# Performance work log

Measured on AMD Instinct MI355X. Metric: run time of the kernel, lower is better.

## Reference

```python
import jax, jax.numpy as jnp
import numpy as np

B, N, NFEAT = 32, 512, 256
NHID, NHEADS, NOUT = 64, 8, 128
ALPHA = 0.2    # GraphAttn LeakyReLU slope
ACVT_SLOPE = 0.01  # default nn.LeakyReLU slope in GAT.acvt
EPS = 1e-12


def _leaky(x, slope):
    return jnp.where(x >= 0, x, slope * x)


def setup_inputs() -> dict:
    key = jax.random.key(0)
    ks = jax.random.split(key, 10)
    s = lambda fan_in: 1.0 / np.sqrt(fan_in)
    return {
        "batch_descs": jax.random.normal(ks[0], (B, N, NFEAT), dtype=jnp.float32),
        # per-head GraphAttn params (nn.Linear weights, no bias)
        "W_tran": jax.random.uniform(ks[1], (NHEADS, NHID, NFEAT), jnp.float32, -s(NFEAT), s(NFEAT)),
        "a1": jax.random.uniform(ks[2], (NHEADS, NHID), jnp.float32, -s(NHID), s(NHID)),
        "a2": jax.random.uniform(ks[3], (NHEADS, NHID), jnp.float32, -s(NHID), s(NHID)),
        # output GraphAttn: in = NHID*NHEADS, out = NOUT
        "W_out": jax.random.uniform(ks[4], (NOUT, NHID * NHEADS), jnp.float32, -s(NHID * NHEADS), s(NHID * NHEADS)),
        "a1_out": jax.random.uniform(ks[5], (NOUT,), jnp.float32, -s(NOUT), s(NOUT)),
        "a2_out": jax.random.uniform(ks[6], (NOUT,), jnp.float32, -s(NOUT), s(NOUT)),
        # final nn.Linear(nout, nout) with bias
        "W_lin": jax.random.uniform(ks[7], (NOUT, NOUT), jnp.float32, -s(NOUT), s(NOUT)),
        "b_lin": jax.random.uniform(ks[8], (NOUT,), jnp.float32, -s(NOUT), s(NOUT)),
    }


def reference(batch_descs, W_tran, a1, a2, W_out, a1_out, a2_out, W_lin, b_lin):
    def gat_one_object(x):  # x: [N, NFEAT]; dense all-ones adj (ignored by GraphAttn)
        # ---- multi-head GraphAttn ----
        h = jnp.einsum('nf,hdf->hnd', x, W_tran)          # [H, N, NHID]
        e1 = jnp.einsum('hnd,hd->hn', h, a1)              # [H, N]
        e2 = jnp.einsum('hnd,hd->hn', h, a2)              # [H, N]
        # e[h, j, k] = a1(h_k) + a2(h_j); softmax over k (torch dim=1 on [N,N])
        e = _leaky(e1[:, None, :] + e2[:, :, None], ALPHA)  # [H, N, N]
        att = jax.nn.softmax(e, axis=-1)
        o = jnp.einsum('hjk,hkd->hjd', att, h)            # [H, N, NHID]
        o = jnp.transpose(o, (1, 0, 2)).reshape(N, NHEADS * NHID)  # concat heads
        # ---- acvt (dropout2 is identity in eval) ----
        x2 = _leaky(o, ACVT_SLOPE)
        # ---- output GraphAttn ----
        h2 = x2 @ W_out.T                                 # [N, NOUT]
        f1 = h2 @ a1_out                                  # [N]
        f2 = h2 @ a2_out                                  # [N]
        e_o = _leaky(f1[None, :] + f2[:, None], ALPHA)    # [N, N]
        att_o = jax.nn.softmax(e_o, axis=-1)
        out = att_o @ h2                                  # [N, NOUT]
        out = jnp.mean(out, axis=0)                       # [NOUT]
        return out @ W_lin.T + b_lin

    feats = jax.vmap(gat_one_object)(batch_descs)         # [B, NOUT]
    # F.normalize(p=2, dim=-1) with eps clamp
    norm = jnp.maximum(jnp.linalg.norm(feats, axis=-1, keepdims=True), EPS)
    return feats / norm
```

## Files before the change

### kernel.cpp

```cpp
#include <hip/hip_runtime.h>
#include <hip/hip_bf16.h>
#include <math.h>

#define BB 32
#define NN 512
#define NF 256
#define NHID 64
#define NHEADS_ 8
#define NO 128
#define ALPHA 0.2f
#define ACVT 0.01f

typedef __attribute__((ext_vector_type(8))) __bf16 bf16x8;
typedef __attribute__((ext_vector_type(4))) __bf16 bf16x4;
typedef __attribute__((ext_vector_type(4))) float f32x4;

__global__ __launch_bounds__(256) void cvt_k(const float* __restrict__ X,
                                             const float* __restrict__ Wt,
                                             const float* __restrict__ Wo,
                                             __bf16* __restrict__ Xb,
                                             __bf16* __restrict__ Wtb,
                                             __bf16* __restrict__ Wob) {
    int u = blockIdx.x * 256 + threadIdx.x;
    const float* src;
    __bf16* dst;
    int idx;
    if (u < 524288) { src = X; dst = Xb; idx = u; }
    else if (u < 540672) { src = Wt; dst = Wtb; idx = u - 524288; }
    else { src = Wo; dst = Wob; idx = u - 540672; }
    float4 v0 = *(const float4*)(src + (size_t)idx * 8);
    float4 v1 = *(const float4*)(src + (size_t)idx * 8 + 4);
    bf16x8 o;
    o[0] = (__bf16)v0.x; o[1] = (__bf16)v0.y; o[2] = (__bf16)v0.z; o[3] = (__bf16)v0.w;
    o[4] = (__bf16)v1.x; o[5] = (__bf16)v1.y; o[6] = (__bf16)v1.z; o[7] = (__bf16)v1.w;
    *(bf16x8*)(dst + (size_t)idx * 8) = o;
}

__global__ __launch_bounds__(256) void gemm1_bf16(
    const __bf16* __restrict__ Xb, const __bf16* __restrict__ Wtb,
    __bf16* __restrict__ HT,
    const float* __restrict__ a1, const float* __restrict__ a2,
    float* __restrict__ E1, float* __restrict__ E2) {
    __shared__ char As[128 * 128];
    __shared__ char Bs[128 * 128];
    const int tid = threadIdx.x;
    const int w = tid >> 6, lane = tid & 63;
    const int wm = w >> 1, wn = w & 1;
    const int r = lane & 15, g = lane >> 4;
    const int m0 = blockIdx.x * 128;
    const int n0 = blockIdx.y * 128;

    f32x4 acc[4][4];
#pragma unroll
    for (int mt = 0; mt < 4; ++mt)
#pragma unroll
        for (int nt = 0; nt < 4; ++nt) {
            acc[mt][nt][0] = 0.f; acc[mt][nt][1] = 0.f;
            acc[mt][nt][2] = 0.f; acc[mt][nt][3] = 0.f;
        }

    const int sr = tid >> 3;
    const int sc = (tid & 7) * 16;

    for (int k0 = 0; k0 < 256; k0 += 64) {
        __syncthreads();
#pragma unroll
        for (int i = 0; i < 4; ++i) {
            int row = sr + i * 32;
            bf16x8 va = *(const bf16x8*)((const char*)Xb +
                                         ((size_t)(m0 + row) * 256 + k0) * 2 + sc);
            *(bf16x8*)(As + row * 128 + (sc ^ ((row & 7) << 4))) = va;
            bf16x8 vb = *(const bf16x8*)((const char*)Wtb +
                                         ((size_t)(n0 + row) * 256 + k0) * 2 + sc);
            *(bf16x8*)(Bs + row * 128 + (sc ^ ((row & 7) << 4))) = vb;
        }
        __syncthreads();
#pragma unroll
        for (int kk = 0; kk < 64; kk += 32) {
            bf16x8 af[4], bfv[4];
#pragma unroll
            for (int mt = 0; mt < 4; ++mt) {
                int row = wm * 64 + mt * 16 + r;
                af[mt] = *(const bf16x8*)(As + row * 128 +
                                          (((kk + g * 8) * 2) ^ ((row & 7) << 4)));
            }
#pragma unroll
            for (int nt = 0; nt < 4; ++nt) {
                int row = wn * 64 + nt * 16 + r;
                bfv[nt] = *(const bf16x8*)(Bs + row * 128 +
                                           (((kk + g * 8) * 2) ^ ((row & 7) << 4)));
            }
#pragma unroll
            for (int mt = 0; mt < 4; ++mt)
#pragma unroll
                for (int nt = 0; nt < 4; ++nt)
                    acc[mt][nt] = __builtin_amdgcn_mfma_f32_16x16x32_bf16(
                        af[mt], bfv[nt], acc[mt][nt], 0, 0, 0);
        }
    }

    const int h = blockIdx.y * 2 + wn;
#pragma unroll
    for (int mt = 0; mt < 4; ++mt) {
        int mfirst = m0 + wm * 64 + mt * 16 + g * 4;
        int b = mfirst >> 9, nn = mfirst & 511;
#pragma unroll
        for (int nt = 0; nt < 4; ++nt) {
            int d = wn * 64 + nt * 16 + r - wn * 64;
            bf16x4 pv;
#pragma unroll
            for (int reg = 0; reg < 4; ++reg) pv[reg] = (__bf16)acc[mt][nt][reg];
            *(bf16x4*)(HT + ((size_t)(b * 8 + h) * 64 + d) * 512 + nn) = pv;
        }
    }
    float w1[4], w2[4];
#pragma unroll
    for (int nt = 0; nt < 4; ++nt) {
        w1[nt] = a1[h * 64 + nt * 16 + r];
        w2[nt] = a2[h * 64 + nt * 16 + r];
    }
#pragma unroll
    for (int mt = 0; mt < 4; ++mt)
#pragma unroll
        for (int reg = 0; reg < 4; ++reg) {
            float s1 = 0.f, s2 = 0.f;
#pragma unroll
            for (int nt = 0; nt < 4; ++nt) {
                s1 += acc[mt][nt][reg] * w1[nt];
                s2 += acc[mt][nt][reg] * w2[nt];
            }
#pragma unroll
            for (int off = 1; off <= 8; off <<= 1) {
                s1 += __shfl_xor(s1, off, 64);
                s2 += __shfl_xor(s2, off, 64);
            }
            if (r == 0) {
                int m = m0 + wm * 64 + mt * 16 + g * 4 + reg;
                int b = m >> 9, n = m & 511;
                E1[(size_t)(b * 8 + h) * 512 + n] = s1;
                E2[(size_t)(b * 8 + h) * 512 + n] = s2;
            }
        }
}

__global__ __launch_bounds__(256) void attn_mfma(const __bf16* __restrict__ HT,
                                                 const float* __restrict__ E1,
                                                 const float* __restrict__ E2,
                                                 __bf16* __restrict__ OL) {
    __shared__ char Ht[64 * 1024];
    __shared__ float e1s[512];
    __shared__ float red[4][64];
    __shared__ float e1maxS;

    const int bid = blockIdx.x;
    const int bh = bid >> 1, half = bid & 1;
    const int b = bh >> 3, h = bh & 7;
    const int tid = threadIdx.x;
    const int w = tid >> 6, lane = tid & 63;
    const int r = lane & 15, g = lane >> 4;

    {
        const char* src = (const char*)(HT + (size_t)bh * 32768);
#pragma unroll
        for (int i = 0; i < 16; ++i) {
            int off = i * 4096 + tid * 16;
            int d = off >> 10;
            bf16x8 v = *(const bf16x8*)(src + off);
            *(bf16x8*)(Ht + (off ^ ((d & 7) << 4))) = v;
        }
    }
    for (int i = tid; i < 512; i += 256) e1s[i] = E1[(size_t)bh * 512 + i];
    __syncthreads();

    ((float*)red)[tid] = fmaxf(e1s[tid], e1s[tid + 256]);
    __syncthreads();
    if (tid < 64) {
        const float* rp = (const float*)red;
        float m = fmaxf(fmaxf(rp[tid], rp[tid + 64]), fmaxf(rp[tid + 128], rp[tid + 192]));
#pragma unroll
        for (int off = 32; off >= 1; off >>= 1) m = fmaxf(m, __shfl_xor(m, off, 64));
        if (tid == 0) e1maxS = m;
    }
    __syncthreads();
    const float e1max = e1maxS;

    float ee2[4], mm[4];
    const float* e2g = E2 + (size_t)bh * 512 + half * 256 + w * 64;
#pragma unroll
    for (int mt = 0; mt < 4; ++mt) {
        float v = e2g[mt * 16 + r];
        ee2[mt] = v;
        float s = e1max + v;
        mm[mt] = fmaxf(s, ALPHA * s);
    }

    f32x4 acc[4][4];
#pragma unroll
    for (int mt = 0; mt < 4; ++mt)
#pragma unroll
        for (int nt = 0; nt < 4; ++nt) {
            acc[mt][nt][0] = 0.f; acc[mt][nt][1] = 0.f;
            acc[mt][nt][2] = 0.f; acc[mt][nt][3] = 0.f;
        }
    float zac[4] = {0.f, 0.f, 0.f, 0.f};

    for (int c = 0; c < 16; ++c) {
        const float* ep = e1s + c * 32 + g * 8;
        float4 ea = *(const float4*)(ep);
        float4 eb = *(const float4*)(ep + 4);
        float e1c[8] = {ea.x, ea.y, ea.z, ea.w, eb.x, eb.y, eb.z, eb.w};

        bf16x8 bfr[4];
#pragma unroll
        for (int nt = 0; nt < 4; ++nt) {
            int n = nt * 16 + r;
            int off = (n << 10) + ((c * 32 + g * 8) << 1);
            off ^= (n & 7) << 4;
            bfr[nt] = *(const bf16x8*)(Ht + off);
        }
#pragma unroll
        for (int mt = 0; mt < 4; ++mt) {
            bf16x8 af;
            float zp = 0.f;
#pragma unroll
            for (int q = 0; q < 8; ++q) {
                float s = e1c[q] + ee2[mt];
                s = fmaxf(s, ALPHA * s);
                float p = __expf(s - mm[mt]);
                zp += p;
                af[q] = (__bf16)p;
            }
            zac[mt] += zp;
#pragma unroll
            for (int nt = 0; nt < 4; ++nt)
                acc[mt][nt] =
                    __builtin_amdgcn_mfma_f32_16x16x32_bf16(af, bfr[nt], acc[mt][nt], 0, 0, 0);
        }
    }

#pragma unroll
    for (int mt = 0; mt < 4; ++mt) {
        float z = zac[mt];
        z += __shfl_xor(z, 16, 64);
        z += __shfl_xor(z, 32, 64);
        if (g == 0) red[w][mt * 16 + r] = 1.f / z;
    }

    __bf16* ob = OL + ((size_t)b * 512 + half * 256 + w * 64) * 512 + h * 64;
#pragma unroll
    for (int mt = 0; mt < 4; ++mt) {
#pragma unroll
        for (int reg = 0; reg < 4; ++reg) {
            int row = mt * 16 + g * 4 + reg;
            float zi = red[w][row];
#pragma unroll
            for (int nt = 0; nt < 4; ++nt) {
                float v = acc[mt][nt][reg] * zi;
                v = fmaxf(v, ACVT * v);
                ob[(size_t)row * 512 + nt * 16 + r] = (__bf16)v;
            }
        }
    }
}

__global__ __launch_bounds__(256) void gemm2_bf16(
    const __bf16* __restrict__ OL, const __bf16* __restrict__ Wob,
    float* __restrict__ H2,
    const float* __restrict__ a1o, const float* __restrict__ a2o,
    float* __restrict__ F1, float* __restrict__ F2) {
    __shared__ char As[32 * 128];
    __shared__ char Bs[128 * 128];
    __shared__ float fred[2][32][2];
    const int tid = threadIdx.x;
    const int w = tid >> 6, lane = tid & 63;
    const int wm = w >> 1, wn = w & 1;
    const int r = lane & 15, g = lane >> 4;
    const int m0 = blockIdx.x * 32;

    f32x4 acc[4];
#pragma unroll
    for (int nt = 0; nt < 4; ++nt) {
        acc[nt][0] = 0.f; acc[nt][1] = 0.f; acc[nt][2] = 0.f; acc[nt][3] = 0.f;
    }

    const int sra = tid >> 3;
    const int sc = (tid & 7) * 16;

    for (int k0 = 0; k0 < 512; k0 += 64) {
        __syncthreads();
        {
            bf16x8 va = *(const bf16x8*)((const char*)OL +
                                         ((size_t)(m0 + sra) * 512 + k0) * 2 + sc);
            *(bf16x8*)(As + sra * 128 + (sc ^ ((sra & 7) << 4))) = va;
        }
#pragma unroll
        for (int i = 0; i < 4; ++i) {
            int row = sra + i * 32;
            bf16x8 vb = *(const bf16x8*)((const char*)Wob +
                                         ((size_t)row * 512 + k0) * 2 + sc);
            *(bf16x8*)(Bs + row * 128 + (sc ^ ((row & 7) << 4))) = vb;
        }
        __syncthreads();
#pragma unroll
        for (int kk = 0; kk < 64; kk += 32) {
            int arow = wm * 16 + r;
            bf16x8 af = *(const bf16x8*)(As + arow * 128 +
                                         (((kk + g * 8) * 2) ^ ((arow & 7) << 4)));
            bf16x8 bfv[4];
#pragma unroll
            for (int nt = 0; nt < 4; ++nt) {
                int row = wn * 64 + nt * 16 + r;
                bfv[nt] = *(const bf16x8*)(Bs + row * 128 +
                                           (((kk + g * 8) * 2) ^ ((row & 7) << 4)));
            }
#pragma unroll
            for (int nt = 0; nt < 4; ++nt)
                acc[nt] = __builtin_amdgcn_mfma_f32_16x16x32_bf16(af, bfv[nt], acc[nt], 0, 0, 0);
        }
    }

#pragma unroll
    for (int reg = 0; reg < 4; ++reg) {
        int row = m0 + wm * 16 + g * 4 + reg;
#pragma unroll
        for (int nt = 0; nt < 4; ++nt)
            H2[(size_t)row * 128 + wn * 64 + nt * 16 + r] = acc[nt][reg];
    }
    float w1[4], w2[4];
#pragma unroll
    for (int nt = 0; nt < 4; ++nt) {
        w1[nt] = a1o[wn * 64 + nt * 16 + r];
        w2[nt] = a2o[wn * 64 + nt * 16 + r];
    }
#pragma unroll
    for (int reg = 0; reg < 4; ++reg) {
        float s1 = 0.f, s2 = 0.f;
#pragma unroll
        for (int nt = 0; nt < 4; ++nt) {
            s1 += acc[nt][reg] * w1[nt];
            s2 += acc[nt][reg] * w2[nt];
        }
#pragma unroll
        for (int off = 1; off <= 8; off <<= 1) {
            s1 += __shfl_xor(s1, off, 64);
            s2 += __shfl_xor(s2, off, 64);
        }
        if (r == 0) {
            int lr = wm * 16 + g * 4 + reg;
            fred[wn][lr][0] = s1;
            fred[wn][lr][1] = s2;
        }
    }
    __syncthreads();
    if (tid < 32) {
        int m = m0 + tid;
        int b = m >> 9, n = m & 511;
        F1[(size_t)b * 512 + n] = fred[0][tid][0] + fred[1][tid][0];
        F2[(size_t)b * 512 + n] = fred[0][tid][1] + fred[1][tid][1];
    }
}

__global__ __launch_bounds__(256) void zw_k(const float* __restrict__ F1,
                                            const float* __restrict__ F2,
                                            float* __restrict__ WP) {
    __shared__ float f1s[512];
    __shared__ float wpart[4][512];
    __shared__ float redm[256];
    const int b = blockIdx.x >> 4, jc = blockIdx.x & 15;
    const int tid = threadIdx.x;
    const int w = tid >> 6, lane = tid & 63;

    f1s[tid] = F1[(size_t)b * 512 + tid];
    f1s[tid + 256] = F1[(size_t)b * 512 + tid + 256];
#pragma unroll
    for (int i = 0; i < 8; ++i) wpart[w][lane + 64 * i] = 0.f;
    __syncthreads();
    redm[tid] = fmaxf(f1s[tid], f1s[tid + 256]);
    __syncthreads();
    if (tid < 64) {
        float m = fmaxf(fmaxf(redm[tid], redm[tid + 64]), fmaxf(redm[tid + 128], redm[tid + 192]));
#pragma unroll
        for (int off = 32; off >= 1; off >>= 1) m = fmaxf(m, __shfl_xor(m, off, 64));
        if (tid == 0) redm[0] = m;
    }
    __syncthreads();
    const float f1m = redm[0];

    for (int jj = 0; jj < 8; ++jj) {
        int j = jc * 32 + w * 8 + jj;
        float f2j = F2[(size_t)b * 512 + j];
        float sj = f1m + f2j;
        float mj = fmaxf(sj, ALPHA * sj);
        float pv[8];
        float z = 0.f;
#pragma unroll
        for (int i = 0; i < 8; ++i) {
            float s = f1s[lane + 64 * i] + f2j;
            s = fmaxf(s, ALPHA * s);
            float p = __expf(s - mj);
            pv[i] = p;
            z += p;
        }
#pragma unroll
        for (int off = 32; off >= 1; off >>= 1) z += __shfl_xor(z, off, 64);
        float inv = 1.f / z;
#pragma unroll
        for (int i = 0; i < 8; ++i) wpart[w][lane + 64 * i] += pv[i] * inv;
    }
    __syncthreads();
    for (int i = tid; i < 512; i += 256)
        WP[(size_t)(b * 16 + jc) * 512 + i] =
            wpart[0][i] + wpart[1][i] + wpart[2][i] + wpart[3][i];
}

__global__ __launch_bounds__(256) void vpart_k(const float* __restrict__ WP,
                                               const float* __restrict__ H2,
                                               float* __restrict__ VP) {
    __shared__ float wsL[128];
    const int b = blockIdx.x, kq = blockIdx.y;
    const int tid = threadIdx.x;
    if (tid < 128) {
        float s = 0.f;
#pragma unroll
        for (int jc = 0; jc < 16; ++jc) s += WP[(size_t)(b * 16 + jc) * 512 + kq * 128 + tid];
        wsL[tid] = s;
    }
    __syncthreads();
    const int d = tid & 127, half = tid >> 7;
    const float* h2p = H2 + ((size_t)b * 512 + kq * 128 + half * 64) * 128 + d;
    float acc = 0.f;
#pragma unroll 8
    for (int i = 0; i < 64; ++i) acc += wsL[half * 64 + i] * h2p[(size_t)i * 128];
    VP[(size_t)(b * 8 + kq * 2 + half) * 128 + d] = acc;
}

__global__ __launch_bounds__(256) void final3_k(const float* __restrict__ VP,
                                                const float* __restrict__ Wl,
                                                const float* __restrict__ bl,
                                                float* __restrict__ out) {
    __shared__ float vs[128];
    __shared__ float fo_s[128];
    __shared__ float r0;
    const int b = blockIdx.x, tid = threadIdx.x;
    if (tid < 128) {
        float v = 0.f;
#pragma unroll
        for (int q = 0; q < 8; ++q) v += VP[(size_t)(b * 8 + q) * 128 + tid];
        vs[tid] = v * (1.f / 512.f);
    }
    __syncthreads();
    if (tid < 128) {
        float fo = bl[tid];
        const float* wl = Wl + (size_t)tid * 128;
#pragma unroll 4
        for (int d = 0; d < 128; d += 4)
            fo += vs[d] * wl[d] + vs[d + 1] * wl[d + 1] + vs[d + 2] * wl[d + 2] +
                  vs[d + 3] * wl[d + 3];
        fo_s[tid] = fo;
    }
    __syncthreads();
    if (tid < 64) {
        float s = fo_s[tid] * fo_s[tid] + fo_s[tid + 64] * fo_s[tid + 64];
#pragma unroll
        for (int off = 32; off >= 1; off >>= 1) s += __shfl_xor(s, off, 64);
        if (tid == 0) r0 = s;
    }
    __syncthreads();
    float inv = 1.f / fmaxf(sqrtf(r0), 1e-12f);
    if (tid < 128) out[(size_t)b * 128 + tid] = fo_s[tid] * inv;
}

extern "C" void kernel_launch(void* const* d_in, const int* in_sizes, int n_in,
                              void* d_out, int out_size, void* d_ws, size_t ws_size,
                              hipStream_t stream) {
    const float* X = (const float*)d_in[0];
    const float* Wt = (const float*)d_in[1];
    const float* a1 = (const float*)d_in[2];
    const float* a2 = (const float*)d_in[3];
    const float* Wo = (const float*)d_in[4];
    const float* a1o = (const float*)d_in[5];
    const float* a2o = (const float*)d_in[6];
    const float* Wl = (const float*)d_in[7];
    const float* bl = (const float*)d_in[8];
    float* out = (float*)d_out;

    char* p = (char*)d_ws;
    __bf16* Xb = (__bf16*)p;  p += (size_t)4194304 * 2;
    __bf16* Wtb = (__bf16*)p; p += (size_t)131072 * 2;
    __bf16* Wob = (__bf16*)p; p += (size_t)65536 * 2;
    __bf16* HT = (__bf16*)p;  p += (size_t)8388608 * 2;
    __bf16* OL = (__bf16*)p;  p += (size_t)8388608 * 2;
    float* E1 = (float*)p;    p += (size_t)131072 * 4;
    float* E2 = (float*)p;    p += (size_t)131072 * 4;
    float* H2 = (float*)p;    p += (size_t)2097152 * 4;
    float* F1 = (float*)p;    p += (size_t)16384 * 4;
    float* F2 = (float*)p;    p += (size_t)16384 * 4;
    float* WP = (float*)p;    p += (size_t)262144 * 4;
    float* VP = (float*)p;    p += (size_t)32768 * 4;

    cvt_k<<<2144, 256, 0, stream>>>(X, Wt, Wo, Xb, Wtb, Wob);
    gemm1_bf16<<<dim3(128, 4), 256, 0, stream>>>(Xb, Wtb, HT, a1, a2, E1, E2);
    attn_mfma<<<512, 256, 0, stream>>>(HT, E1, E2, OL);
    gemm2_bf16<<<512, 256, 0, stream>>>(OL, Wob, H2, a1o, a2o, F1, F2);
    zw_k<<<512, 256, 0, stream>>>(F1, F2, WP);
    vpart_k<<<dim3(32, 4), 256, 0, stream>>>(WP, H2, VP);
    final3_k<<<32, 256, 0, stream>>>(VP, Wl, bl, out);
}
```

Before: 146.2 us.

## Fuse bf16 conversion into GEMM loads, stream H from global, merge final kernels

Removes the separate fp32-to-bf16 conversion kernel: the two GEMMs now read fp32 inputs and weights directly and convert them while staging into shared memory. The attention kernel no longer copies its full 64KB H tile into LDS. Instead each wave register-prefetches the next chunk of B fragments from global memory. The vpart and final kernels are merged into one 512-thread kernel per batch. Together this cuts two launches and an extra round trip of X through memory, at the cost of doubled fp32 load bytes in gemm1 and global-latency-bound B fragments in attention, which may have worse reuse than LDS.

```diff
diff --git a/kernel.cpp b/kernel.cpp
--- a/kernel.cpp
+++ b/kernel.cpp
@@ -2,12 +2,6 @@
 #include <hip/hip_bf16.h>
 #include <math.h>
 
-#define BB 32
-#define NN 512
-#define NF 256
-#define NHID 64
-#define NHEADS_ 8
-#define NO 128
 #define ALPHA 0.2f
 #define ACVT 0.01f
 
@@ -15,29 +9,17 @@
 typedef __attribute__((ext_vector_type(4))) __bf16 bf16x4;
 typedef __attribute__((ext_vector_type(4))) float f32x4;
 
-__global__ __launch_bounds__(256) void cvt_k(const float* __restrict__ X,
-                                             const float* __restrict__ Wt,
-                                             const float* __restrict__ Wo,
-                                             __bf16* __restrict__ Xb,
-                                             __bf16* __restrict__ Wtb,
-                                             __bf16* __restrict__ Wob) {
-    int u = blockIdx.x * 256 + threadIdx.x;
-    const float* src;
-    __bf16* dst;
-    int idx;
-    if (u < 524288) { src = X; dst = Xb; idx = u; }
-    else if (u < 540672) { src = Wt; dst = Wtb; idx = u - 524288; }
-    else { src = Wo; dst = Wob; idx = u - 540672; }
-    float4 v0 = *(const float4*)(src + (size_t)idx * 8);
-    float4 v1 = *(const float4*)(src + (size_t)idx * 8 + 4);
+__device__ __forceinline__ bf16x8 cvt8(const float* p) {
+    float4 v0 = *(const float4*)p;
+    float4 v1 = *(const float4*)(p + 4);
     bf16x8 o;
     o[0] = (__bf16)v0.x; o[1] = (__bf16)v0.y; o[2] = (__bf16)v0.z; o[3] = (__bf16)v0.w;
     o[4] = (__bf16)v1.x; o[5] = (__bf16)v1.y; o[6] = (__bf16)v1.z; o[7] = (__bf16)v1.w;
-    *(bf16x8*)(dst + (size_t)idx * 8) = o;
-}
-
-__global__ __launch_bounds__(256) void gemm1_bf16(
-    const __bf16* __restrict__ Xb, const __bf16* __restrict__ Wtb,
+    return o;
+}
+
+__global__ __launch_bounds__(256) void gemm1_f(
+    const float* __restrict__ X, const float* __restrict__ Wt,
     __bf16* __restrict__ HT,
     const float* __restrict__ a1, const float* __restrict__ a2,
     float* __restrict__ E1, float* __restrict__ E2) {
@@ -60,19 +42,17 @@
         }
 
     const int sr = tid >> 3;
-    const int sc = (tid & 7) * 16;
+    const int c8 = (tid & 7) * 8;
 
     for (int k0 = 0; k0 < 256; k0 += 64) {
         __syncthreads();
 #pragma unroll
         for (int i = 0; i < 4; ++i) {
             int row = sr + i * 32;
-            bf16x8 va = *(const bf16x8*)((const char*)Xb +
-                                         ((size_t)(m0 + row) * 256 + k0) * 2 + sc);
-            *(bf16x8*)(As + row * 128 + (sc ^ ((row & 7) << 4))) = va;
-            bf16x8 vb = *(const bf16x8*)((const char*)Wtb +
-                                         ((size_t)(n0 + row) * 256 + k0) * 2 + sc);
-            *(bf16x8*)(Bs + row * 128 + (sc ^ ((row & 7) << 4))) = vb;
+            bf16x8 va = cvt8(X + (size_t)(m0 + row) * 256 + k0 + c8);
+            *(bf16x8*)(As + row * 128 + ((c8 * 2) ^ ((row & 7) << 4))) = va;
+            bf16x8 vb = cvt8(Wt + (size_t)(n0 + row) * 256 + k0 + c8);
+            *(bf16x8*)(Bs + row * 128 + ((c8 * 2) ^ ((row & 7) << 4))) = vb;
         }
         __syncthreads();
 #pragma unroll
@@ -106,7 +86,7 @@
         int b = mfirst >> 9, nn = mfirst & 511;
 #pragma unroll
         for (int nt = 0; nt < 4; ++nt) {
-            int d = wn * 64 + nt * 16 + r - wn * 64;
+            int d = nt * 16 + r;
             bf16x4 pv;
 #pragma unroll
             for (int reg = 0; reg < 4; ++reg) pv[reg] = (__bf16)acc[mt][nt][reg];
@@ -143,11 +123,10 @@
         }
 }
 
-__global__ __launch_bounds__(256) void attn_mfma(const __bf16* __restrict__ HT,
-                                                 const float* __restrict__ E1,
-                                                 const float* __restrict__ E2,
-                                                 __bf16* __restrict__ OL) {
-    __shared__ char Ht[64 * 1024];
+__global__ __launch_bounds__(256) void attn_g(const __bf16* __restrict__ HT,
+                                              const float* __restrict__ E1,
+                                              const float* __restrict__ E2,
+                                              __bf16* __restrict__ OL) {
     __shared__ float e1s[512];
     __shared__ float red[4][64];
     __shared__ float e1maxS;
@@ -159,16 +138,6 @@
     const int w = tid >> 6, lane = tid & 63;
     const int r = lane & 15, g = lane >> 4;
 
-    {
-        const char* src = (const char*)(HT + (size_t)bh * 32768);
-#pragma unroll
-        for (int i = 0; i < 16; ++i) {
-            int off = i * 4096 + tid * 16;
-            int d = off >> 10;
-            bf16x8 v = *(const bf16x8*)(src + off);
-            *(bf16x8*)(Ht + (off ^ ((d & 7) << 4))) = v;
-        }
-    }
     for (int i = tid; i < 512; i += 256) e1s[i] = E1[(size_t)bh * 512 + i];
     __syncthreads();
 
@@ -204,20 +173,24 @@
         }
     float zac[4] = {0.f, 0.f, 0.f, 0.f};
 
+    const __bf16* hb = HT + (size_t)bh * 32768;
+    bf16x8 cur[4], nxt[4];
+#pragma unroll
+    for (int nt = 0; nt < 4; ++nt)
+        cur[nt] = *(const bf16x8*)(hb + (size_t)(nt * 16 + r) * 512 + g * 8);
+
     for (int c = 0; c < 16; ++c) {
+        if (c < 15) {
+#pragma unroll
+            for (int nt = 0; nt < 4; ++nt)
+                nxt[nt] = *(const bf16x8*)(hb + (size_t)(nt * 16 + r) * 512 +
+                                           (c + 1) * 32 + g * 8);
+        }
         const float* ep = e1s + c * 32 + g * 8;
         float4 ea = *(const float4*)(ep);
         float4 eb = *(const float4*)(ep + 4);
         float e1c[8] = {ea.x, ea.y, ea.z, ea.w, eb.x, eb.y, eb.z, eb.w};
 
-        bf16x8 bfr[4];
-#pragma unroll
-        for (int nt = 0; nt < 4; ++nt) {
-            int n = nt * 16 + r;
-            int off = (n << 10) + ((c * 32 + g * 8) << 1);
-            off ^= (n & 7) << 4;
-            bfr[nt] = *(const bf16x8*)(Ht + off);
-        }
 #pragma unroll
         for (int mt = 0; mt < 4; ++mt) {
             bf16x8 af;
@@ -234,7 +207,11 @@
 #pragma unroll
             for (int nt = 0; nt < 4; ++nt)
                 acc[mt][nt] =
-                    __builtin_amdgcn_mfma_f32_16x16x32_bf16(af, bfr[nt], acc[mt][nt], 0, 0, 0);
+                    __builtin_amdgcn_mfma_f32_16x16x32_bf16(af, cur[nt], acc[mt][nt], 0, 0, 0);
+        }
+        if (c < 15) {
+#pragma unroll
+            for (int nt = 0; nt < 4; ++nt) cur[nt] = nxt[nt];
         }
     }
 
@@ -263,8 +240,8 @@
     }
 }
 
-__global__ __launch_bounds__(256) void gemm2_bf16(
-    const __bf16* __restrict__ OL, const __bf16* __restrict__ Wob,
+__global__ __launch_bounds__(256) void gemm2_f(
+    const __bf16* __restrict__ OL, const float* __restrict__ Wo,
     float* __restrict__ H2,
     const float* __restrict__ a1o, const float* __restrict__ a2o,
     float* __restrict__ F1, float* __restrict__ F2) {
@@ -284,21 +261,20 @@
     }
 
     const int sra = tid >> 3;
-    const int sc = (tid & 7) * 16;
+    const int c8 = (tid & 7) * 8;
 
     for (int k0 = 0; k0 < 512; k0 += 64) {
         __syncthreads();
         {
             bf16x8 va = *(const bf16x8*)((const char*)OL +
-                                         ((size_t)(m0 + sra) * 512 + k0) * 2 + sc);
-            *(bf16x8*)(As + sra * 128 + (sc ^ ((sra & 7) << 4))) = va;
+                                         ((size_t)(m0 + sra) * 512 + k0) * 2 + c8 * 2);
+            *(bf16x8*)(As + sra * 128 + ((c8 * 2) ^ ((sra & 7) << 4))) = va;
         }
 #pragma unroll
         for (int i = 0; i < 4; ++i) {
             int row = sra + i * 32;
-            bf16x8 vb = *(const bf16x8*)((const char*)Wob +
-                                         ((size_t)row * 512 + k0) * 2 + sc);
-            *(bf16x8*)(Bs + row * 128 + (sc ^ ((row & 7) << 4))) = vb;
+            bf16x8 vb = cvt8(Wo + (size_t)row * 512 + k0 + c8);
+            *(bf16x8*)(Bs + row * 128 + ((c8 * 2) ^ ((row & 7) << 4))) = vb;
         }
         __syncthreads();
 #pragma unroll
@@ -413,41 +389,35 @@
             wpart[0][i] + wpart[1][i] + wpart[2][i] + wpart[3][i];
 }
 
-__global__ __launch_bounds__(256) void vpart_k(const float* __restrict__ WP,
-                                               const float* __restrict__ H2,
-                                               float* __restrict__ VP) {
-    __shared__ float wsL[128];
-    const int b = blockIdx.x, kq = blockIdx.y;
-    const int tid = threadIdx.x;
-    if (tid < 128) {
-        float s = 0.f;
-#pragma unroll
-        for (int jc = 0; jc < 16; ++jc) s += WP[(size_t)(b * 16 + jc) * 512 + kq * 128 + tid];
-        wsL[tid] = s;
-    }
-    __syncthreads();
-    const int d = tid & 127, half = tid >> 7;
-    const float* h2p = H2 + ((size_t)b * 512 + kq * 128 + half * 64) * 128 + d;
-    float acc = 0.f;
-#pragma unroll 8
-    for (int i = 0; i < 64; ++i) acc += wsL[half * 64 + i] * h2p[(size_t)i * 128];
-    VP[(size_t)(b * 8 + kq * 2 + half) * 128 + d] = acc;
-}
-
-__global__ __launch_bounds__(256) void final3_k(const float* __restrict__ VP,
+__global__ __launch_bounds__(512) void finalv_k(const float* __restrict__ WP,
+                                                const float* __restrict__ H2,
                                                 const float* __restrict__ Wl,
                                                 const float* __restrict__ bl,
                                                 float* __restrict__ out) {
+    __shared__ float wsL[512];
+    __shared__ float part[4][128];
     __shared__ float vs[128];
     __shared__ float fo_s[128];
     __shared__ float r0;
     const int b = blockIdx.x, tid = threadIdx.x;
-    if (tid < 128) {
-        float v = 0.f;
-#pragma unroll
-        for (int q = 0; q < 8; ++q) v += VP[(size_t)(b * 8 + q) * 128 + tid];
-        vs[tid] = v * (1.f / 512.f);
-    }
+    {
+        float s = 0.f;
+#pragma unroll
+        for (int jc = 0; jc < 16; ++jc) s += WP[(size_t)(b * 16 + jc) * 512 + tid];
+        wsL[tid] = s;
+    }
+    __syncthreads();
+    {
+        const int q = tid >> 7, d = tid & 127;
+        const float* h2p = H2 + ((size_t)b * 512 + q * 128) * 128 + d;
+        float acc = 0.f;
+#pragma unroll 8
+        for (int i = 0; i < 128; ++i) acc += wsL[q * 128 + i] * h2p[(size_t)i * 128];
+        part[q][d] = acc;
+    }
+    __syncthreads();
+    if (tid < 128)
+        vs[tid] = (part[0][tid] + part[1][tid] + part[2][tid] + part[3][tid]) * (1.f / 512.f);
     __syncthreads();
     if (tid < 128) {
         float fo = bl[tid];
@@ -485,9 +455,6 @@
     float* out = (float*)d_out;
 
     char* p = (char*)d_ws;
-    __bf16* Xb = (__bf16*)p;  p += (size_t)4194304 * 2;
-    __bf16* Wtb = (__bf16*)p; p += (size_t)131072 * 2;
-    __bf16* Wob = (__bf16*)p; p += (size_t)65536 * 2;
     __bf16* HT = (__bf16*)p;  p += (size_t)8388608 * 2;
     __bf16* OL = (__bf16*)p;  p += (size_t)8388608 * 2;
     float* E1 = (float*)p;    p += (size_t)131072 * 4;
@@ -496,13 +463,10 @@
     float* F1 = (float*)p;    p += (size_t)16384 * 4;
     float* F2 = (float*)p;    p += (size_t)16384 * 4;
     float* WP = (float*)p;    p += (size_t)262144 * 4;
-    float* VP = (float*)p;    p += (size_t)32768 * 4;
-
-    cvt_k<<<2144, 256, 0, stream>>>(X, Wt, Wo, Xb, Wtb, Wob);
-    gemm1_bf16<<<dim3(128, 4), 256, 0, stream>>>(Xb, Wtb, HT, a1, a2, E1, E2);
-    attn_mfma<<<512, 256, 0, stream>>>(HT, E1, E2, OL);
-    gemm2_bf16<<<512, 256, 0, stream>>>(OL, Wob, H2, a1o, a2o, F1, F2);
+
+    gemm1_f<<<dim3(128, 4), 256, 0, stream>>>(X, Wt, HT, a1, a2, E1, E2);
+    attn_g<<<512, 256, 0, stream>>>(HT, E1, E2, OL);
+    gemm2_f<<<512, 256, 0, stream>>>(OL, Wo, H2, a1o, a2o, F1, F2);
     zw_k<<<512, 256, 0, stream>>>(F1, F2, WP);
-    vpart_k<<<dim3(32, 4), 256, 0, stream>>>(WP, H2, VP);
-    final3_k<<<32, 256, 0, stream>>>(VP, Wl, bl, out);
-}
+    finalv_k<<<32, 512, 0, stream>>>(WP, H2, Wl, bl, out);
+}
```

Result: no change. 146.3 us (+0.0%).
